# Kernel tuning notes

Measured on AMD Instinct MI355X. Metric: run time of the kernel, lower is better.

Reference implementation:

```python
import jax, jax.numpy as jnp
import numpy as np

B, C_IN, C_MID, HW, EMB, N_ATTR = 512, 1024, 512, 14, 1024, 8
BN_EPS = 1e-5


def setup_inputs() -> dict:
    key = jax.random.key(0)
    ks = jax.random.split(key, 20)
    s = lambda *sh: 1.0 / np.sqrt(sh[-1])
    return {
        "x": jax.random.normal(ks[0], (B, C_IN, HW, HW), jnp.float32),
        "c": jax.random.randint(ks[1], (B,), 0, N_ATTR),
        "attr_emb": jax.random.normal(ks[2], (N_ATTR, 512), jnp.float32),
        "Wt1": jax.random.normal(ks[3], (512, 512), jnp.float32) * s(512, 512),
        "bt1": jnp.zeros((512,), jnp.float32),
        "Wc": jax.random.normal(ks[4], (C_MID, C_IN), jnp.float32) * s(C_MID, C_IN),
        "bc": jnp.zeros((C_MID,), jnp.float32),
        "bn_gamma": jnp.ones((C_MID,), jnp.float32),
        "bn_beta": jnp.zeros((C_MID,), jnp.float32),
        "bn_mean": jnp.zeros((C_MID,), jnp.float32),
        "bn_var": jax.random.uniform(ks[5], (C_MID,), jnp.float32, 0.5, 1.5),
        "Wt2": jax.random.normal(ks[6], (512, 512), jnp.float32) * s(512, 512),
        "bt2": jnp.zeros((512,), jnp.float32),
        "W1": jax.random.normal(ks[7], (512, 1536), jnp.float32) * s(512, 1536),
        "b1": jnp.zeros((512,), jnp.float32),
        "W2": jax.random.normal(ks[8], (1024, 512), jnp.float32) * s(1024, 512),
        "b2": jnp.zeros((1024,), jnp.float32),
        "Wf": jax.random.normal(ks[9], (EMB, 1024), jnp.float32) * s(EMB, 1024),
        "bf": jnp.zeros((EMB,), jnp.float32),
    }


def reference(x, c, attr_emb, Wt1, bt1, Wc, bc, bn_gamma, bn_beta, bn_mean, bn_var,
              Wt2, bt2, W1, b1, W2, b2, Wf, bf):
    # conv1 (1x1) + BN (inference stats) + tanh -> img: [B, 512, 14, 14]
    img = jnp.einsum('bchw,oc->bohw', x, Wc) + bc[None, :, None, None]
    inv_std = jax.lax.rsqrt(bn_var + BN_EPS)
    img = (img - bn_mean[None, :, None, None]) * (bn_gamma * inv_std)[None, :, None, None] \
          + bn_beta[None, :, None, None]
    img = jnp.tanh(img)
    # attribute query: [B, 512]
    emb = attr_emb[c]
    attr = jnp.tanh(emb @ Wt1.T + bt1)
    # attention map: channel dot product, scale, spatial softmax
    attmap = jnp.einsum('bk,bkhw->bhw', attr, img) / np.sqrt(512.0)  # [B,14,14]
    attmap = jax.nn.softmax(attmap.reshape(B, -1), axis=-1).reshape(B, HW, HW)
    # attended feature: [B, 1024]
    feat = jnp.einsum('bchw,bhw->bc', x, attmap)
    # gated fusion
    attr2 = jax.nn.relu(emb @ Wt2.T + bt2)
    img_attr = jnp.concatenate([feat, attr2], axis=1)  # [B, 1536]
    mask = jax.nn.sigmoid(jax.nn.relu(img_attr @ W1.T + b1) @ W2.T + b2)
    out = (feat * mask) @ Wf.T + bf  # [B, EMB]
    # l2norm over dim 1
    norm = jnp.sqrt(jnp.sum(out * out, axis=1, keepdims=True))
    return out / norm
```

## Files before the change

### kernel.cpp

```cpp
#include <hip/hip_runtime.h>
#include <hip/hip_bf16.h>
#include <math.h>

#define HW2 196
#define CIN 1024

using f32x4 = __attribute__((ext_vector_type(4))) float;
using s16x8 = __attribute__((ext_vector_type(8))) short;

__device__ __forceinline__ float tanh_fast(float x) {
  float cx = fminf(fmaxf(x, -15.f), 15.f);
  float e = __expf(2.f * cx);
  return (e - 1.f) / (e + 1.f);
}

__device__ __forceinline__ unsigned int pkbf(float a, float b) {
  union { __hip_bfloat162 h; unsigned int u; } v;
  v.h = __float22bfloat162_rn(make_float2(a, b));
  return v.u;
}

__global__ void k_pre1(const float* __restrict__ attr_emb,
                       const float* __restrict__ Wt1, const float* __restrict__ bt1,
                       const float* __restrict__ Wt2, const float* __restrict__ bt2,
                       const float* __restrict__ bc, const float* __restrict__ gamma,
                       const float* __restrict__ beta, const float* __restrict__ mean,
                       const float* __restrict__ var,
                       float* __restrict__ attr1_tab, float* __restrict__ attr2_tab,
                       float* __restrict__ bnA, float* __restrict__ bnB) {
  int gid = blockIdx.x * 256 + threadIdx.x;
  if (gid < 4096) {
    int a = gid >> 9, j = gid & 511;
    const float* e = attr_emb + a * 512;
    const float* w1 = Wt1 + j * 512;
    const float* w2 = Wt2 + j * 512;
    float d1 = 0.f, d2 = 0.f;
    for (int i = 0; i < 512; ++i) {
      float ev = e[i];
      d1 += ev * w1[i];
      d2 += ev * w2[i];
    }
    attr1_tab[gid] = tanh_fast(d1 + bt1[j]);
    float r = d2 + bt2[j];
    attr2_tab[gid] = r > 0.f ? r : 0.f;
  } else if (gid < 4608) {
    int o = gid - 4096;
    float A = gamma[o] * rsqrtf(var[o] + 1e-5f);
    bnA[o] = A;
    bnB[o] = (bc[o] - mean[o]) * A + beta[o];
  }
}

__global__ void k_pre2(const float* __restrict__ W1, const float* __restrict__ b1,
                       const float* __restrict__ attr2_tab, float* __restrict__ t2,
                       const float* __restrict__ Wc, unsigned short* __restrict__ wcbf) {
  int bid = blockIdx.x;
  if (bid < 16) {
    int gid = bid * 256 + threadIdx.x;
    int a = gid >> 9, j = gid & 511;
    const float* w = W1 + (size_t)j * 1536 + 1024;
    const float* at = attr2_tab + a * 512;
    float d = 0.f;
    for (int i = 0; i < 512; ++i) d += w[i] * at[i];
    t2[gid] = d + b1[j];
  } else {
    int idx = (bid - 16) * 256 + threadIdx.x;
    const float* src = Wc + (size_t)idx * 16;
    f32x4 a0 = *(const f32x4*)src;
    f32x4 a1 = *(const f32x4*)(src + 4);
    f32x4 a2 = *(const f32x4*)(src + 8);
    f32x4 a3 = *(const f32x4*)(src + 12);
    unsigned int* dp = (unsigned int*)&wcbf[(size_t)idx * 16];
    dp[0] = pkbf(a0.x, a0.y); dp[1] = pkbf(a0.z, a0.w);
    dp[2] = pkbf(a1.x, a1.y); dp[3] = pkbf(a1.z, a1.w);
    dp[4] = pkbf(a2.x, a2.y); dp[5] = pkbf(a2.z, a2.w);
    dp[6] = pkbf(a3.x, a3.y); dp[7] = pkbf(a3.z, a3.w);
  }
}

__global__ __launch_bounds__(256, 2) void k_main(
    const float* __restrict__ x, const unsigned short* __restrict__ wcbf,
    const int* __restrict__ cidx, const float* __restrict__ attr1_tab,
    const float* __restrict__ bnA, const float* __restrict__ bnB,
    float* __restrict__ feat) {
  __shared__ __align__(16) unsigned short Xt[208 * 72];
  __shared__ __align__(16) unsigned short Wl[128 * 72];
  __shared__ float attr_l[512], bnA_l[512], bnB_l[512];
  __shared__ float s_lds[HW2];
  __shared__ float red[8];

  int b = blockIdx.x, tid = threadIdx.x;
  int wid = tid >> 6, lane = tid & 63, quad = lane >> 4, l15 = lane & 15;

  int ca = cidx[b];
  for (int i = tid; i < 512; i += 256) {
    attr_l[i] = attr1_tab[ca * 512 + i];
    bnA_l[i] = bnA[i];
    bnB_l[i] = bnB[i];
  }
  {
    unsigned int* zp = (unsigned int*)&Xt[196 * 72];
    for (int i = tid; i < 432; i += 256) zp[i] = 0u;
  }

  const float* xb = x + (size_t)b * (CIN * HW2);
  int t0 = wid * 3;
  int ntile = (wid == 3) ? 4 : 3;

  float sv[4][4];
#pragma unroll
  for (int mt = 0; mt < 4; ++mt)
#pragma unroll
    for (int r = 0; r < 4; ++r) sv[mt][r] = 0.f;

  for (int och = 0; och < 4; ++och) {
    int o_base = och * 128;
    f32x4 acc[4][8];
#pragma unroll
    for (int mt = 0; mt < 4; ++mt)
#pragma unroll
      for (int q = 0; q < 8; ++q) {
        f32x4 z = {0.f, 0.f, 0.f, 0.f};
        acc[mt][q] = z;
      }
    for (int kt = 0; kt < 16; ++kt) {
      __syncthreads();
      int c0 = kt * 64;
      const float* xs = xb + (size_t)c0 * HW2;
#pragma unroll
      for (int it = 0; it < 4; ++it) {
        int id = it * 256 + tid;
        if (id < 784) {
          int cq = id / 49;
          int hw4 = id - cq * 49;
          const float* p = xs + (size_t)cq * (4 * HW2) + hw4 * 4;
          f32x4 v0 = *(const f32x4*)p;
          f32x4 v1 = *(const f32x4*)(p + HW2);
          f32x4 v2 = *(const f32x4*)(p + 2 * HW2);
          f32x4 v3 = *(const f32x4*)(p + 3 * HW2);
          int s = (hw4 & 7) << 1;
          int ub = (cq ^ s) << 2;
#pragma unroll
          for (int r = 0; r < 4; ++r) {
            unsigned long long wv =
                (unsigned long long)pkbf(v0[r], v1[r]) |
                ((unsigned long long)pkbf(v2[r], v3[r]) << 32);
            *(unsigned long long*)&Xt[(hw4 * 4 + r) * 72 + ub] = wv;
          }
        }
      }
#pragma unroll
      for (int it = 0; it < 4; ++it) {
        int ch = it * 256 + tid;
        int row = ch >> 3, u = ch & 7;
        s16x8 v = *(const s16x8*)&wcbf[(size_t)(o_base + row) * CIN + c0 + u * 8];
        *(s16x8*)&Wl[row * 72 + u * 8] = v;
      }
      __syncthreads();
#pragma unroll
      for (int kk = 0; kk < 2; ++kk) {
        s16x8 af[4];
#pragma unroll
        for (int mt = 0; mt < 4; ++mt)
          if (mt < ntile) {
            int hw = (t0 + mt) * 16 + l15;
            int s = ((hw >> 2) & 7) << 1;
            int u = (kk << 3) + (quad << 1);
            af[mt] = *(const s16x8*)&Xt[hw * 72 + ((u ^ s) << 2)];
          }
#pragma unroll
        for (int h = 0; h < 2; ++h) {
          s16x8 bfr[4];
#pragma unroll
          for (int nt = 0; nt < 4; ++nt)
            bfr[nt] = *(const s16x8*)&Wl[(h * 64 + nt * 16 + l15) * 72 + kk * 32 + quad * 8];
#pragma unroll
          for (int mt = 0; mt < 4; ++mt)
            if (mt < ntile) {
#pragma unroll
              for (int nt = 0; nt < 4; ++nt)
                acc[mt][h * 4 + nt] = __builtin_amdgcn_mfma_f32_16x16x32_bf16(
                    af[mt], bfr[nt], acc[mt][h * 4 + nt], 0, 0, 0);
            }
        }
      }
    }
    float at[8], sa[8], sb[8];
#pragma unroll
    for (int q = 0; q < 8; ++q) {
      int o = o_base + q * 16 + l15;
      at[q] = attr_l[o]; sa[q] = bnA_l[o]; sb[q] = bnB_l[o];
    }
#pragma unroll
    for (int mt = 0; mt < 4; ++mt)
      if (mt < ntile) {
#pragma unroll
        for (int r = 0; r < 4; ++r) {
          float v = 0.f;
#pragma unroll
          for (int q = 0; q < 8; ++q)
            v += at[q] * tanh_fast(acc[mt][q][r] * sa[q] + sb[q]);
          sv[mt][r] += v;
        }
      }
  }
#pragma unroll
  for (int mt = 0; mt < 4; ++mt)
    if (mt < ntile) {
#pragma unroll
      for (int r = 0; r < 4; ++r) {
        float v = sv[mt][r];
        v += __shfl_xor(v, 1);
        v += __shfl_xor(v, 2);
        v += __shfl_xor(v, 4);
        v += __shfl_xor(v, 8);
        int hw = (t0 + mt) * 16 + quad * 4 + r;
        if (l15 == 0 && hw < HW2) s_lds[hw] = v;
      }
    }
  __syncthreads();
  {
    float v = (tid < HW2) ? s_lds[tid] * 0.04419417382415922f : -1e30f;
    float m = v;
    for (int off = 32; off > 0; off >>= 1) m = fmaxf(m, __shfl_xor(m, off));
    if (lane == 0) red[wid] = m;
    __syncthreads();
    float gm = fmaxf(fmaxf(red[0], red[1]), fmaxf(red[2], red[3]));
    float e = (tid < HW2) ? __expf(v - gm) : 0.f;
    float s = e;
    for (int off = 32; off > 0; off >>= 1) s += __shfl_xor(s, off);
    __syncthreads();
    if (lane == 0) red[wid] = s;
    __syncthreads();
    float gs = red[0] + red[1] + red[2] + red[3];
    if (tid < HW2) s_lds[tid] = e / gs;
  }
  __syncthreads();
  for (int cc = tid; cc < 1024; cc += 256) {
    const float* xr = xb + (size_t)cc * HW2;
    float a = 0.f;
#pragma unroll
    for (int h4 = 0; h4 < 49; ++h4) {
      f32x4 v = *(const f32x4*)(xr + h4 * 4);
      a += s_lds[h4 * 4 + 0] * v.x + s_lds[h4 * 4 + 1] * v.y +
           s_lds[h4 * 4 + 2] * v.z + s_lds[h4 * 4 + 3] * v.w;
    }
    feat[(size_t)b * 1024 + cc] = a;
  }
}

__device__ __forceinline__ void dot8(const float* __restrict__ w,
                                     const float* __restrict__ fa, const float* __restrict__ fb,
                                     int i, float& a0, float& a1) {
  f32x4 wa = *(const f32x4*)(w + i);
  f32x4 wb = *(const f32x4*)(w + i + 4);
  a0 += wa.x * fa[i+0]; a1 += wa.x * fb[i+0];
  a0 += wa.y * fa[i+1]; a1 += wa.y * fb[i+1];
  a0 += wa.z * fa[i+2]; a1 += wa.z * fb[i+2];
  a0 += wa.w * fa[i+3]; a1 += wa.w * fb[i+3];
  a0 += wb.x * fa[i+4]; a1 += wb.x * fb[i+4];
  a0 += wb.y * fa[i+5]; a1 += wb.y * fb[i+5];
  a0 += wb.z * fa[i+6]; a1 += wb.z * fb[i+6];
  a0 += wb.w * fa[i+7]; a1 += wb.w * fb[i+7];
}

__global__ __launch_bounds__(512) void k_mlp(
    const float* __restrict__ feat, const int* __restrict__ cidx, const float* __restrict__ t2,
    const float* __restrict__ W1, const float* __restrict__ W2,
    const float* __restrict__ b2, const float* __restrict__ Wf,
    const float* __restrict__ bfb, float* __restrict__ out) {
  __shared__ float f0[1024], f1[1024];
  __shared__ float h0[512], h1[512];
  __shared__ float g0[1024], g1[1024];
  __shared__ float red[16];
  int tid = threadIdx.x;
  int b0 = blockIdx.x * 2, b1 = b0 + 1;
  int c0 = cidx[b0], c1 = cidx[b1];
  for (int i = tid; i < 1024; i += 512) {
    f0[i] = feat[(size_t)b0 * 1024 + i];
    f1[i] = feat[(size_t)b1 * 1024 + i];
  }
  __syncthreads();
  {
    int j = tid;
    const float* w = W1 + (size_t)j * 1536;
    float a0 = 0.f, a1 = 0.f;
    for (int i = 0; i < 1024; i += 8) dot8(w, f0, f1, i, a0, a1);
    h0[j] = fmaxf(a0 + t2[c0 * 512 + j], 0.f);
    h1[j] = fmaxf(a1 + t2[c1 * 512 + j], 0.f);
  }
  __syncthreads();
  for (int m = tid; m < 1024; m += 512) {
    const float* w = W2 + (size_t)m * 512;
    float a0 = 0.f, a1 = 0.f;
    for (int i = 0; i < 512; i += 8) dot8(w, h0, h1, i, a0, a1);
    float bb = b2[m];
    float s0 = 1.f / (1.f + __expf(-(a0 + bb)));
    float s1 = 1.f / (1.f + __expf(-(a1 + bb)));
    g0[m] = f0[m] * s0;
    g1[m] = f1[m] * s1;
  }
  __syncthreads();
  float o0[2], o1[2];
  float ss0 = 0.f, ss1 = 0.f;
#pragma unroll
  for (int t = 0; t < 2; ++t) {
    int e = tid + t * 512;
    const float* w = Wf + (size_t)e * 1024;
    float a0 = 0.f, a1 = 0.f;
    for (int i = 0; i < 1024; i += 8) dot8(w, g0, g1, i, a0, a1);
    float bb = bfb[e];
    a0 += bb; a1 += bb;
    o0[t] = a0; o1[t] = a1;
    ss0 += a0 * a0; ss1 += a1 * a1;
  }
  for (int off = 32; off > 0; off >>= 1) {
    ss0 += __shfl_xor(ss0, off);
    ss1 += __shfl_xor(ss1, off);
  }
  int wid = tid >> 6, lane = tid & 63;
  if (lane == 0) { red[wid] = ss0; red[wid + 8] = ss1; }
  __syncthreads();
  float t0 = 0.f, t1 = 0.f;
#pragma unroll
  for (int w = 0; w < 8; ++w) { t0 += red[w]; t1 += red[w + 8]; }
  float n0 = rsqrtf(t0), n1 = rsqrtf(t1);
#pragma unroll
  for (int t = 0; t < 2; ++t) {
    int e = tid + t * 512;
    out[(size_t)b0 * 1024 + e] = o0[t] * n0;
    out[(size_t)b1 * 1024 + e] = o1[t] * n1;
  }
}

extern "C" void kernel_launch(void* const* d_in, const int* in_sizes, int n_in,
                              void* d_out, int out_size, void* d_ws, size_t ws_size,
                              hipStream_t stream) {
  const float* x        = (const float*)d_in[0];
  const int*   c        = (const int*)d_in[1];
  const float* attr_emb = (const float*)d_in[2];
  const float* Wt1      = (const float*)d_in[3];
  const float* bt1      = (const float*)d_in[4];
  const float* Wc       = (const float*)d_in[5];
  const float* bc       = (const float*)d_in[6];
  const float* gamma    = (const float*)d_in[7];
  const float* beta     = (const float*)d_in[8];
  const float* mean     = (const float*)d_in[9];
  const float* var      = (const float*)d_in[10];
  const float* Wt2      = (const float*)d_in[11];
  const float* bt2      = (const float*)d_in[12];
  const float* W1       = (const float*)d_in[13];
  const float* b1       = (const float*)d_in[14];
  const float* W2       = (const float*)d_in[15];
  const float* b2       = (const float*)d_in[16];
  const float* Wf       = (const float*)d_in[17];
  const float* bfb      = (const float*)d_in[18];

  char* ws = (char*)d_ws;
  float* feat      = (float*)ws;
  float* attr1_tab = (float*)(ws + 2097152);
  float* attr2_tab = attr1_tab + 4096;
  float* t2        = attr2_tab + 4096;
  float* bnA       = t2 + 4096;
  float* bnB       = bnA + 512;
  unsigned short* wcbf = (unsigned short*)(ws + 2150400);

  hipLaunchKernelGGL(k_pre1, dim3(18), dim3(256), 0, stream,
                     attr_emb, Wt1, bt1, Wt2, bt2, bc, gamma, beta, mean, var,
                     attr1_tab, attr2_tab, bnA, bnB);
  hipLaunchKernelGGL(k_pre2, dim3(144), dim3(256), 0, stream,
                     W1, b1, attr2_tab, t2, Wc, wcbf);
  hipLaunchKernelGGL(k_main, dim3(512), dim3(256), 0, stream,
                     x, wcbf, c, attr1_tab, bnA, bnB, feat);
  hipLaunchKernelGGL(k_mlp, dim3(256), dim3(512), 0, stream,
                     feat, c, t2, W1, W2, b2, Wf, bfb, (float*)d_out);
}
```

Baseline: 1.217 ms.

## Double-buffer x tiles via async global-to-LDS loads, read weights from global

Replaces the synchronous x staging (global load, bf16 pack, swizzled LDS store) with direct global_load_lds async copies of raw fp32 x into a double-buffered LDS tile of 32 channels. The next tile is prefetched while the current one is used, and the och/kt loops are flattened into one pipelined loop. The weight fragments are now read directly from global memory instead of through LDS. The bf16 conversion moves into the fragment load, which does strided scalar LDS reads that may cause bank conflicts. The fp32 tiles use more LDS, which could limit occupancy.

```diff
diff --git a/kernel.cpp b/kernel.cpp
--- a/kernel.cpp
+++ b/kernel.cpp
@@ -18,6 +18,12 @@
   union { __hip_bfloat162 h; unsigned int u; } v;
   v.h = __float22bfloat162_rn(make_float2(a, b));
   return v.u;
+}
+
+__device__ __forceinline__ void gload_lds16(const void* g, void* l) {
+  __builtin_amdgcn_global_load_lds(
+      (const __attribute__((address_space(1))) void*)(void*)g,
+      (__attribute__((address_space(3))) void*)l, 16, 0, 0);
 }
 
 __global__ void k_pre1(const float* __restrict__ attr_emb,
@@ -83,8 +89,7 @@
     const int* __restrict__ cidx, const float* __restrict__ attr1_tab,
     const float* __restrict__ bnA, const float* __restrict__ bnB,
     float* __restrict__ feat) {
-  __shared__ __align__(16) unsigned short Xt[208 * 72];
-  __shared__ __align__(16) unsigned short Wl[128 * 72];
+  __shared__ __align__(16) float Xt[2][32 * HW2];
   __shared__ float attr_l[512], bnA_l[512], bnB_l[512];
   __shared__ float s_lds[HW2];
   __shared__ float red[8];
@@ -98,10 +103,6 @@
     bnA_l[i] = bnA[i];
     bnB_l[i] = bnB[i];
   }
-  {
-    unsigned int* zp = (unsigned int*)&Xt[196 * 72];
-    for (int i = tid; i < 432; i += 256) zp[i] = 0u;
-  }
 
   const float* xb = x + (size_t)b * (CIN * HW2);
   int t0 = wid * 3;
@@ -113,97 +114,92 @@
 #pragma unroll
     for (int r = 0; r < 4; ++r) sv[mt][r] = 0.f;
 
-  for (int och = 0; och < 4; ++och) {
-    int o_base = och * 128;
-    f32x4 acc[4][8];
+  auto stage = [&](int c0, int bsel) {
+    const char* gs = (const char*)(xb + (size_t)c0 * HW2);
+    char* ls = (char*)&Xt[bsel][0];
+    for (int slot = wid; slot < 25; slot += 4) {
+      int off = slot * 1024 + lane * 16;
+      if (off < 25088) gload_lds16(gs + off, ls + off);
+    }
+  };
+
+  f32x4 acc[4][8];
+
+  stage(0, 0);
+  __syncthreads();
+
+  for (int t = 0; t < 128; ++t) {
+    int kt = t & 31, c0 = kt * 32;
+    int och = t >> 5, o_base = och * 128;
+    if (kt == 0) {
+#pragma unroll
+      for (int mt = 0; mt < 4; ++mt)
+#pragma unroll
+        for (int q = 0; q < 8; ++q) {
+          f32x4 z = {0.f, 0.f, 0.f, 0.f};
+          acc[mt][q] = z;
+        }
+    }
+    if (t + 1 < 128) stage(((t + 1) & 31) * 32, (t + 1) & 1);
+
+    const float* Xb = &Xt[t & 1][0];
+    s16x8 af[4];
 #pragma unroll
     for (int mt = 0; mt < 4; ++mt)
+      if (mt < ntile) {
+        int hw = (t0 + mt) * 16 + l15;
+        int hwc = hw < 195 ? hw : 195;
+        float msk = (hw < HW2) ? 1.f : 0.f;
+        const float* base = Xb + quad * 8 * HW2 + hwc;
+        float xv[8];
+#pragma unroll
+        for (int j = 0; j < 8; ++j) xv[j] = base[j * HW2] * msk;
+        union { unsigned int u[4]; s16x8 s; } cv;
+        cv.u[0] = pkbf(xv[0], xv[1]);
+        cv.u[1] = pkbf(xv[2], xv[3]);
+        cv.u[2] = pkbf(xv[4], xv[5]);
+        cv.u[3] = pkbf(xv[6], xv[7]);
+        af[mt] = cv.s;
+      }
+#pragma unroll
+    for (int h = 0; h < 2; ++h) {
+      s16x8 bfr[4];
+#pragma unroll
+      for (int nt = 0; nt < 4; ++nt)
+        bfr[nt] = *(const s16x8*)&wcbf[(size_t)(o_base + h * 64 + nt * 16 + l15) * CIN +
+                                       c0 + quad * 8];
+#pragma unroll
+      for (int mt = 0; mt < 4; ++mt)
+        if (mt < ntile) {
+#pragma unroll
+          for (int nt = 0; nt < 4; ++nt)
+            acc[mt][h * 4 + nt] = __builtin_amdgcn_mfma_f32_16x16x32_bf16(
+                af[mt], bfr[nt], acc[mt][h * 4 + nt], 0, 0, 0);
+        }
+    }
+    if (kt == 31) {
+      float at[8], sa[8], sb[8];
 #pragma unroll
       for (int q = 0; q < 8; ++q) {
-        f32x4 z = {0.f, 0.f, 0.f, 0.f};
-        acc[mt][q] = z;
+        int o = o_base + q * 16 + l15;
+        at[q] = attr_l[o]; sa[q] = bnA_l[o]; sb[q] = bnB_l[o];
       }
-    for (int kt = 0; kt < 16; ++kt) {
-      __syncthreads();
-      int c0 = kt * 64;
-      const float* xs = xb + (size_t)c0 * HW2;
-#pragma unroll
-      for (int it = 0; it < 4; ++it) {
-        int id = it * 256 + tid;
-        if (id < 784) {
-          int cq = id / 49;
-          int hw4 = id - cq * 49;
-          const float* p = xs + (size_t)cq * (4 * HW2) + hw4 * 4;
-          f32x4 v0 = *(const f32x4*)p;
-          f32x4 v1 = *(const f32x4*)(p + HW2);
-          f32x4 v2 = *(const f32x4*)(p + 2 * HW2);
-          f32x4 v3 = *(const f32x4*)(p + 3 * HW2);
-          int s = (hw4 & 7) << 1;
-          int ub = (cq ^ s) << 2;
+#pragma unroll
+      for (int mt = 0; mt < 4; ++mt)
+        if (mt < ntile) {
 #pragma unroll
           for (int r = 0; r < 4; ++r) {
-            unsigned long long wv =
-                (unsigned long long)pkbf(v0[r], v1[r]) |
-                ((unsigned long long)pkbf(v2[r], v3[r]) << 32);
-            *(unsigned long long*)&Xt[(hw4 * 4 + r) * 72 + ub] = wv;
+            float v = 0.f;
+#pragma unroll
+            for (int q = 0; q < 8; ++q)
+              v += at[q] * tanh_fast(acc[mt][q][r] * sa[q] + sb[q]);
+            sv[mt][r] += v;
           }
         }
-      }
-#pragma unroll
-      for (int it = 0; it < 4; ++it) {
-        int ch = it * 256 + tid;
-        int row = ch >> 3, u = ch & 7;
-        s16x8 v = *(const s16x8*)&wcbf[(size_t)(o_base + row) * CIN + c0 + u * 8];
-        *(s16x8*)&Wl[row * 72 + u * 8] = v;
-      }
-      __syncthreads();
-#pragma unroll
-      for (int kk = 0; kk < 2; ++kk) {
-        s16x8 af[4];
-#pragma unroll
-        for (int mt = 0; mt < 4; ++mt)
-          if (mt < ntile) {
-            int hw = (t0 + mt) * 16 + l15;
-            int s = ((hw >> 2) & 7) << 1;
-            int u = (kk << 3) + (quad << 1);
-            af[mt] = *(const s16x8*)&Xt[hw * 72 + ((u ^ s) << 2)];
-          }
-#pragma unroll
-        for (int h = 0; h < 2; ++h) {
-          s16x8 bfr[4];
-#pragma unroll
-          for (int nt = 0; nt < 4; ++nt)
-            bfr[nt] = *(const s16x8*)&Wl[(h * 64 + nt * 16 + l15) * 72 + kk * 32 + quad * 8];
-#pragma unroll
-          for (int mt = 0; mt < 4; ++mt)
-            if (mt < ntile) {
-#pragma unroll
-              for (int nt = 0; nt < 4; ++nt)
-                acc[mt][h * 4 + nt] = __builtin_amdgcn_mfma_f32_16x16x32_bf16(
-                    af[mt], bfr[nt], acc[mt][h * 4 + nt], 0, 0, 0);
-            }
-        }
-      }
-    }
-    float at[8], sa[8], sb[8];
-#pragma unroll
-    for (int q = 0; q < 8; ++q) {
-      int o = o_base + q * 16 + l15;
-      at[q] = attr_l[o]; sa[q] = bnA_l[o]; sb[q] = bnB_l[o];
-    }
-#pragma unroll
-    for (int mt = 0; mt < 4; ++mt)
-      if (mt < ntile) {
-#pragma unroll
-        for (int r = 0; r < 4; ++r) {
-          float v = 0.f;
-#pragma unroll
-          for (int q = 0; q < 8; ++q)
-            v += at[q] * tanh_fast(acc[mt][q][r] * sa[q] + sb[q]);
-          sv[mt][r] += v;
-        }
-      }
-  }
+    }
+    __syncthreads();
+  }
+
 #pragma unroll
   for (int mt = 0; mt < 4; ++mt)
     if (mt < ntile) {
```

Result: slower. 1.289 ms (+5.9%).
